# Optimization experiments

Hardware: AMD Instinct MI355X
Metric: run time of the kernel (lower is better)

Reference implementation:

```python
import jax, jax.numpy as jnp
import numpy as np

ALPHA = 0.1
BETA = 0.9

B, S = 512, 32768


def setup_inputs() -> dict:
    key = jax.random.key(0)
    k1, k2 = jax.random.split(key)
    # posterior probabilities strictly inside (0,1) so logs are finite
    posterior = jax.random.uniform(k1, (B, S, 2), dtype=jnp.float32,
                                   minval=0.01, maxval=0.99)
    length = jax.random.randint(k2, (B,), 1, S + 1, dtype=jnp.int64)
    return {"posterior": posterior, "length": length}


def reference(posterior, length):
    alpha = jnp.float32(ALPHA)
    beta = jnp.float32(BETA)
    log_a = jnp.log(alpha)
    log_1a = jnp.log(1.0 - alpha)
    log_b = jnp.log(beta)
    log_1b = jnp.log(1.0 - beta)

    p0 = posterior[..., 0]  # [B, S]
    p1 = posterior[..., 1]  # [B, S]

    # first-timestep KL against the alpha prior (always counted, per original)
    first = p1[:, 0] * (jnp.log(p1[:, 0]) - log_a) \
          + p0[:, 0] * (jnp.log(p0[:, 0]) - log_1a)  # [B]

    # pairwise expected KL between consecutive timesteps, s = 1..S-1
    past0, past1 = p0[:, :-1], p1[:, :-1]   # [B, S-1]
    curr0, curr1 = p0[:, 1:], p1[:, 1:]
    lc0 = jnp.log(curr0)
    lc1 = jnp.log(curr1)
    div = past1 * (curr1 * (lc1 - log_b) + curr0 * (lc0 - log_1b)) \
        + past0 * (curr1 * (lc1 - log_1b) + curr0 * (lc0 - log_b))  # [B, S-1]

    # ragged mask: timestep index s (1-based) contributes iff s < length[b]
    s_idx = jnp.arange(1, p0.shape[1])  # [S-1]
    mask = (s_idx[None, :] < length[:, None]).astype(div.dtype)

    total = first.sum() + (div * mask).sum()
    return total / p0.shape[0]
```

## Files before the change

### kernel.cpp

```cpp
#include <hip/hip_runtime.h>

#define TILE      4096
#define NTHREADS  256
#define PER_ITER  (NTHREADS * 2)

#define L1C (-2.3025850929940457f)
#define L9C (-0.10536051565782628f)

__global__ __launch_bounds__(NTHREADS) void ekl_main(
    const float* __restrict__ posterior,
    const int*   __restrict__ length,
    double*      __restrict__ partial,
    int S, int chunks)
{
    const int b      = blockIdx.y;
    const int chunk  = blockIdx.x;
    const int cstart = chunk * TILE;
    const int tid    = threadIdx.x;
    const int pidx   = b * chunks + chunk;
    const int len    = length[b];

    if (cstart > 0 && cstart >= len) {
        if (tid == 0) partial[pidx] = 0.0;
        return;
    }

    const float* row = posterior + (size_t)b * (size_t)S * 2u;
    float acc = 0.0f;

    #pragma unroll
    for (int j = 0; j < TILE / PER_ITER; ++j) {
        const int s0 = cstart + j * PER_ITER + 2 * tid;
        const bool act = (s0 < len) || (s0 == 0);

        float4 c = make_float4(1.0f, 1.0f, 1.0f, 1.0f);
        if (act) c = *(const float4*)(row + 2 * (size_t)s0);

        float pvx = __shfl_up(c.z, 1, 64);
        float pvy = __shfl_up(c.w, 1, 64);

        if (act) {
            if ((tid & 63) == 0 && s0 > 0) {
                const float2 t = *(const float2*)(row + 2 * (size_t)s0 - 2);
                pvx = t.x; pvy = t.y;
            }

            const float l0x = __logf(c.x), l0y = __logf(c.y);
            const float A0 = c.y * (l0y - L9C) + c.x * (l0x - L1C);
            const float B0 = c.y * (l0y - L1C) + c.x * (l0x - L9C);
            acc += (s0 == 0) ? B0 : (pvy * A0 + pvx * B0);

            if (s0 + 1 < len) {
                const float l1x = __logf(c.z), l1y = __logf(c.w);
                acc += c.y * (c.w * (l1y - L9C) + c.z * (l1x - L1C))
                     + c.x * (c.w * (l1y - L1C) + c.z * (l1x - L9C));
            }
        }
    }

    #pragma unroll
    for (int off = 32; off > 0; off >>= 1)
        acc += __shfl_down(acc, off, 64);

    __shared__ double wsum[NTHREADS / 64];
    if ((tid & 63) == 0) wsum[tid >> 6] = (double)acc;
    __syncthreads();
    if (tid == 0) {
        double t = 0.0;
        #pragma unroll
        for (int i = 0; i < NTHREADS / 64; ++i) t += wsum[i];
        partial[pidx] = t;
    }
}

#define RTHREADS 1024
__global__ __launch_bounds__(RTHREADS) void ekl_reduce(
    const double* __restrict__ partial, int n,
    float* __restrict__ out, double invB)
{
    double acc = 0.0;
    for (int i = threadIdx.x; i < n; i += RTHREADS) acc += partial[i];
    #pragma unroll
    for (int off = 32; off > 0; off >>= 1)
        acc += __shfl_down(acc, off, 64);
    __shared__ double wsum[RTHREADS / 64];
    if ((threadIdx.x & 63) == 0) wsum[threadIdx.x >> 6] = acc;
    __syncthreads();
    if (threadIdx.x == 0) {
        double t = 0.0;
        #pragma unroll
        for (int i = 0; i < RTHREADS / 64; ++i) t += wsum[i];
        out[0] = (float)(t * invB);
    }
}

extern "C" void kernel_launch(void* const* d_in, const int* in_sizes, int n_in,
                              void* d_out, int out_size, void* d_ws, size_t ws_size,
                              hipStream_t stream)
{
    const float* posterior = (const float*)d_in[0];
    const int*   length    = (const int*)d_in[1];

    const int B = in_sizes[1];
    const int S = (int)((long long)in_sizes[0] / ((long long)B * 2));
    const int chunks = (S + TILE - 1) / TILE;

    double* partial = (double*)d_ws;

    dim3 grid(chunks, B);
    ekl_main<<<grid, NTHREADS, 0, stream>>>(posterior, length, partial, S, chunks);
    ekl_reduce<<<1, RTHREADS, 0, stream>>>(partial, B * chunks, (float*)d_out,
                                           1.0 / (double)B);
}
```

Baseline: 188.6 us.

## Fuse final reduction via atomics and process four positions per thread with fast path

```diff
diff --git a/kernel.cpp b/kernel.cpp
--- a/kernel.cpp
+++ b/kernel.cpp
@@ -1,59 +1,97 @@
 #include <hip/hip_runtime.h>
 
-#define TILE      4096
-#define NTHREADS  256
-#define PER_ITER  (NTHREADS * 2)
+#define TILE           4096
+#define NTHREADS       256
+#define POS_PER_THREAD 4
+#define PER_ITER       (NTHREADS * POS_PER_THREAD)
+#define NITER          (TILE / PER_ITER)
+#define NACC           16
 
 #define L1C (-2.3025850929940457f)
 #define L9C (-0.10536051565782628f)
 
+__device__ __forceinline__ void ab(float c0, float c1, float& A, float& B) {
+    const float l0 = __logf(c0), l1 = __logf(c1);
+    A = c1 * (l1 - L9C) + c0 * (l0 - L1C);
+    B = c1 * (l1 - L1C) + c0 * (l0 - L9C);
+}
+
 __global__ __launch_bounds__(NTHREADS) void ekl_main(
     const float* __restrict__ posterior,
     const int*   __restrict__ length,
-    double*      __restrict__ partial,
-    int S, int chunks)
+    void*        __restrict__ ws,
+    float*       __restrict__ out,
+    int S, int nblocks, double invB)
 {
     const int b      = blockIdx.y;
     const int chunk  = blockIdx.x;
     const int cstart = chunk * TILE;
     const int tid    = threadIdx.x;
-    const int pidx   = b * chunks + chunk;
     const int len    = length[b];
 
-    if (cstart > 0 && cstart >= len) {
-        if (tid == 0) partial[pidx] = 0.0;
-        return;
-    }
-
-    const float* row = posterior + (size_t)b * (size_t)S * 2u;
     float acc = 0.0f;
 
-    #pragma unroll
-    for (int j = 0; j < TILE / PER_ITER; ++j) {
-        const int s0 = cstart + j * PER_ITER + 2 * tid;
-        const bool act = (s0 < len) || (s0 == 0);
+    if (cstart < len || cstart == 0) {
+        const float* row = posterior + (size_t)b * (size_t)S * 2u;
 
-        float4 c = make_float4(1.0f, 1.0f, 1.0f, 1.0f);
-        if (act) c = *(const float4*)(row + 2 * (size_t)s0);
+        if (cstart + TILE <= len) {
+            #pragma unroll
+            for (int j = 0; j < NITER; ++j) {
+                const int s0 = cstart + j * PER_ITER + POS_PER_THREAD * tid;
+                const float4 u = *(const float4*)(row + 2 * (size_t)s0);
+                const float4 v = *(const float4*)(row + 2 * (size_t)s0 + 4);
 
-        float pvx = __shfl_up(c.z, 1, 64);
-        float pvy = __shfl_up(c.w, 1, 64);
+                float pvx = __shfl_up(v.z, 1, 64);
+                float pvy = __shfl_up(v.w, 1, 64);
+                if ((tid & 63) == 0 && s0 > 0) {
+                    const float2 t = *(const float2*)(row + 2 * (size_t)s0 - 2);
+                    pvx = t.x; pvy = t.y;
+                }
 
-        if (act) {
-            if ((tid & 63) == 0 && s0 > 0) {
-                const float2 t = *(const float2*)(row + 2 * (size_t)s0 - 2);
-                pvx = t.x; pvy = t.y;
+                float A, B;
+                ab(u.x, u.y, A, B);
+                acc += (s0 == 0) ? B : (pvy * A + pvx * B);
+                ab(u.z, u.w, A, B);
+                acc += u.y * A + u.x * B;
+                ab(v.x, v.y, A, B);
+                acc += u.w * A + u.z * B;
+                ab(v.z, v.w, A, B);
+                acc += v.y * A + v.x * B;
             }
+        } else {
+            #pragma unroll
+            for (int j = 0; j < NITER; ++j) {
+                const int s0 = cstart + j * PER_ITER + POS_PER_THREAD * tid;
+                float4 u = make_float4(1.f, 1.f, 1.f, 1.f);
+                float4 v = make_float4(1.f, 1.f, 1.f, 1.f);
+                const bool a0 = (s0 < len) || (s0 == 0);
+                if (a0)           u = *(const float4*)(row + 2 * (size_t)s0);
+                if (s0 + 2 < len) v = *(const float4*)(row + 2 * (size_t)s0 + 4);
 
-            const float l0x = __logf(c.x), l0y = __logf(c.y);
-            const float A0 = c.y * (l0y - L9C) + c.x * (l0x - L1C);
-            const float B0 = c.y * (l0y - L1C) + c.x * (l0x - L9C);
-            acc += (s0 == 0) ? B0 : (pvy * A0 + pvx * B0);
+                float pvx = __shfl_up(v.z, 1, 64);
+                float pvy = __shfl_up(v.w, 1, 64);
 
-            if (s0 + 1 < len) {
-                const float l1x = __logf(c.z), l1y = __logf(c.w);
-                acc += c.y * (c.w * (l1y - L9C) + c.z * (l1x - L1C))
-                     + c.x * (c.w * (l1y - L1C) + c.z * (l1x - L9C));
+                if (a0) {
+                    if ((tid & 63) == 0 && s0 > 0) {
+                        const float2 t = *(const float2*)(row + 2 * (size_t)s0 - 2);
+                        pvx = t.x; pvy = t.y;
+                    }
+                    float A, B;
+                    ab(u.x, u.y, A, B);
+                    acc += (s0 == 0) ? B : (pvy * A + pvx * B);
+                    if (s0 + 1 < len) {
+                        ab(u.z, u.w, A, B);
+                        acc += u.y * A + u.x * B;
+                    }
+                    if (s0 + 2 < len) {
+                        ab(v.x, v.y, A, B);
+                        acc += u.w * A + u.z * B;
+                        if (s0 + 3 < len) {
+                            ab(v.z, v.w, A, B);
+                            acc += v.y * A + v.x * B;
+                        }
+                    }
+                }
             }
         }
     }
@@ -65,32 +103,26 @@
     __shared__ double wsum[NTHREADS / 64];
     if ((tid & 63) == 0) wsum[tid >> 6] = (double)acc;
     __syncthreads();
+
     if (tid == 0) {
         double t = 0.0;
         #pragma unroll
         for (int i = 0; i < NTHREADS / 64; ++i) t += wsum[i];
-        partial[pidx] = t;
-    }
-}
 
-#define RTHREADS 1024
-__global__ __launch_bounds__(RTHREADS) void ekl_reduce(
-    const double* __restrict__ partial, int n,
-    float* __restrict__ out, double invB)
-{
-    double acc = 0.0;
-    for (int i = threadIdx.x; i < n; i += RTHREADS) acc += partial[i];
-    #pragma unroll
-    for (int off = 32; off > 0; off >>= 1)
-        acc += __shfl_down(acc, off, 64);
-    __shared__ double wsum[RTHREADS / 64];
-    if ((threadIdx.x & 63) == 0) wsum[threadIdx.x >> 6] = acc;
-    __syncthreads();
-    if (threadIdx.x == 0) {
-        double t = 0.0;
-        #pragma unroll
-        for (int i = 0; i < RTHREADS / 64; ++i) t += wsum[i];
-        out[0] = (float)(t * invB);
+        unsigned int* counter = (unsigned int*)ws;
+        double*       accum   = (double*)((char*)ws + 64);
+
+        if (t != 0.0)
+            atomicAdd(&accum[(blockIdx.y * gridDim.x + blockIdx.x) & (NACC - 1)], t);
+        __threadfence();
+        const unsigned int old = atomicAdd(counter, 1u);
+        if (old == (unsigned int)(nblocks - 1)) {
+            double tot = 0.0;
+            #pragma unroll
+            for (int i = 0; i < NACC; ++i)
+                tot += atomicAdd(&accum[i], 0.0);
+            out[0] = (float)(tot * invB);
+        }
     }
 }
 
@@ -104,11 +136,11 @@
     const int B = in_sizes[1];
     const int S = (int)((long long)in_sizes[0] / ((long long)B * 2));
     const int chunks = (S + TILE - 1) / TILE;
+    const int nblocks = chunks * B;
 
-    double* partial = (double*)d_ws;
+    hipMemsetAsync(d_ws, 0, 256, stream);
 
     dim3 grid(chunks, B);
-    ekl_main<<<grid, NTHREADS, 0, stream>>>(posterior, length, partial, S, chunks);
-    ekl_reduce<<<1, RTHREADS, 0, stream>>>(partial, B * chunks, (float*)d_out,
-                                           1.0 / (double)B);
+    ekl_main<<<grid, NTHREADS, 0, stream>>>(posterior, length, d_ws, (float*)d_out,
+                                            S, nblocks, 1.0 / (double)B);
 }
```

Measured after the change: 364.9 us. 93.4% more time.
